# Kernel optimization log

Measured on AMD Instinct MI355X. Metric: run time of the kernel, lower is better.

Reference implementation:

```python
import jax, jax.numpy as jnp
import numpy as np

DIM = 1024
N_QUAT = DIM // 4
LN_EPS = 1e-5
NORM_EPS = 1e-12


def quat_mul(q1, q2):
    # q1, q2: [B, L, N, 4]
    r1, i1, j1, k1 = q1[..., 0], q1[..., 1], q1[..., 2], q1[..., 3]
    r2, i2, j2, k2 = q2[..., 0], q2[..., 1], q2[..., 2], q2[..., 3]
    r = r1 * r2 - i1 * i2 - j1 * j2 - k1 * k2
    i = r1 * i2 + i1 * r2 + j1 * k2 - k1 * j2
    j = r1 * j2 - i1 * k2 + j1 * r2 + k1 * i2
    k = r1 * k2 + i1 * j2 - j1 * i2 + k1 * r2
    return jnp.stack([r, i, j, k], axis=-1)


def quat_conj(q):
    return q * jnp.array([1.0, -1.0, -1.0, -1.0], dtype=q.dtype)


def setup_inputs() -> dict:
    key = jax.random.key(0)
    ks = jax.random.split(key, 7)
    B, L, D = 4, 4096, DIM
    s = 1.0 / np.sqrt(D)
    return {
        "x": jax.random.normal(ks[0], (B, L, D), dtype=jnp.float32),
        "Wk": jax.random.normal(ks[1], (D, D), dtype=jnp.float32) * s,
        "bk": jnp.zeros((D,), dtype=jnp.float32),
        "Wv": jax.random.normal(ks[2], (D, D), dtype=jnp.float32) * s,
        "bv": jnp.zeros((D,), dtype=jnp.float32),
        "ln_g": jnp.ones((D,), dtype=jnp.float32),
        "ln_b": jnp.zeros((D,), dtype=jnp.float32),
        "Wo": jax.random.normal(ks[3], (D, D), dtype=jnp.float32) * s,
        "bo": jnp.zeros((D,), dtype=jnp.float32),
    }


def reference(x, Wk, bk, Wv, bv, ln_g, ln_b, Wo, bo):
    B, L, D = x.shape
    keys = (x @ Wk.T + bk).reshape(B, L, N_QUAT, 4)
    knorm = jnp.linalg.norm(keys, axis=-1, keepdims=True)
    keys = keys / jnp.maximum(knorm, NORM_EPS)  # F.normalize
    values = (x @ Wv.T + bv).reshape(B, L, N_QUAT, 4)
    bound = quat_mul(values, keys)
    memory = jnp.cumsum(bound, axis=1)
    retrieved = quat_mul(memory, quat_conj(keys)).reshape(B, L, D)
    positions = jnp.arange(1, L + 1, dtype=x.dtype)
    retrieved = retrieved / jnp.sqrt(positions)[None, :, None]
    # LayerNorm over last dim
    mu = jnp.mean(retrieved, axis=-1, keepdims=True)
    var = jnp.var(retrieved, axis=-1, keepdims=True)
    normed = (retrieved - mu) / jnp.sqrt(var + LN_EPS) * ln_g + ln_b
    return x + (normed @ Wo.T + bo)
```

## Files before the change

kernel.cpp:

```cpp
#include <hip/hip_runtime.h>
#include <cstdint>
#include <cstddef>


typedef float    f32x4 __attribute__((ext_vector_type(4)));
typedef _Float16 f16x8 __attribute__((ext_vector_type(8)));
typedef _Float16 f16x4 __attribute__((ext_vector_type(4)));

#define DEV static __device__ __forceinline__

constexpr int BATCH = 4;
constexpr int LSEQ  = 4096;
constexpr int DIMN  = 1024;
constexpr int MROW  = BATCH * LSEQ;
constexpr int SEG   = 128;
constexpr int SL    = LSEQ / SEG;
constexpr int NT    = DIMN / 64;

DEV f32x4 qmul(f32x4 a, f32x4 b) {
  f32x4 r;
  r.x = a.x*b.x - a.y*b.y - a.z*b.z - a.w*b.w;
  r.y = a.x*b.y + a.y*b.x + a.z*b.w - a.w*b.z;
  r.z = a.x*b.z - a.y*b.w + a.z*b.x + a.w*b.y;
  r.w = a.x*b.w + a.y*b.z - a.z*b.y + a.w*b.x;
  return r;
}

DEV f32x4 h2f(f16x4 h) {
  return (f32x4){(float)h.x, (float)h.y, (float)h.z, (float)h.w};
}

__global__ __launch_bounds__(256) void k_cast_all(
    const float* __restrict__ x, const float* __restrict__ w0,
    const float* __restrict__ w1, const float* __restrict__ w2,
    _Float16* __restrict__ out) {
  const int XN4 = MROW * DIMN / 4;
  const int WN4 = DIMN * DIMN / 4;
  int i = blockIdx.x * 256 + threadIdx.x;
  if (i >= XN4 + 3 * WN4) return;
  const float* src; int j;
  if (i < XN4)                { src = x;  j = i; }
  else if (i < XN4 + WN4)     { src = w0; j = i - XN4; }
  else if (i < XN4 + 2 * WN4) { src = w1; j = i - XN4 - WN4; }
  else                        { src = w2; j = i - XN4 - 2 * WN4; }
  f32x4 v = ((const f32x4*)src)[j];
  f16x4 o = { (_Float16)v.x, (_Float16)v.y, (_Float16)v.z, (_Float16)v.w };
  ((f16x4*)out)[i] = o;
}

__global__ __launch_bounds__(512, 2) void k_gemm256(
    const _Float16* __restrict__ A, const _Float16* __restrict__ Bw,
    const float* __restrict__ biasA, const float* __restrict__ biasB, int nsplit,
    _Float16* __restrict__ C, int ldC, int nbn) {
  extern __shared__ char smem[];
  const int tid  = threadIdx.x;
  const int lane = tid & 63;
  const int wid  = tid >> 6;
  const int wr = wid >> 2, wc = wid & 3;

  const int nwg = gridDim.x;
  const int cpx = nwg >> 3;
  const int swz = (blockIdx.x & 7) * cpx + (blockIdx.x >> 3);
  const int bm = swz / nbn, bn = swz % nbn;

  auto regBase = [](int slot, int isB, int half) -> unsigned {
    return (unsigned)(((slot * 2 + isB) * 2 + half) * 16384);
  };
  const int r8    = lane >> 3;
  const int sslot = (lane & 7) ^ r8;
  const char* aT = (const char*)(A  + (size_t)bm * 256 * DIMN);
  const char* bT = (const char*)(Bw + (size_t)bn * 256 * DIMN);

  auto stage = [&](int isB, int half, int slot, int kt) {
    const char* gb = (isB ? bT : aT) + (size_t)(half * 128) * 2048 + kt * 128;
    const unsigned reg = regBase(slot, isB, half);
#pragma unroll
    for (int i = 0; i < 2; ++i) {
      const int c = wid * 2 + i;
      const char* src = gb + (size_t)(c * 8 + r8) * 2048 + (sslot << 4);
      __builtin_amdgcn_global_load_lds(
          (const __attribute__((address_space(1))) void*)src,
          (__attribute__((address_space(3))) void*)(smem + reg + c * 1024), 16, 0, 0);
    }
  };
  auto fragA = [&](int slot, int m, int kk) -> f16x8 {
    const int half = m >> 2;
    const int row  = wr * 64 + (m & 3) * 16 + (lane & 15);
    const int sl   = (kk * 4 + (lane >> 4)) ^ (row & 7);
    return *(const f16x8*)(smem + regBase(slot, 0, half) + row * 128 + (sl << 4));
  };
  auto fragB = [&](int slot, int n, int kk) -> f16x8 {
    const int half = n >> 1;
    const int row  = wc * 32 + (n & 1) * 16 + (lane & 15);
    const int sl   = (kk * 4 + (lane >> 4)) ^ (row & 7);
    return *(const f16x8*)(smem + regBase(slot, 1, half) + row * 128 + (sl << 4));
  };

  f32x4 acc[8][4];
#pragma unroll
  for (int m = 0; m < 8; ++m)
#pragma unroll
    for (int n = 0; n < 4; ++n) acc[m][n] = (f32x4){0.f, 0.f, 0.f, 0.f};

  stage(0, 0, 0, 0); stage(1, 0, 0, 0); stage(0, 1, 0, 0); stage(1, 1, 0, 0);

  f16x8 a[4][2], b[4][2];
#pragma unroll 2
  for (int T = 0; T < NT; ++T) {
    const int slot = T & 1, ns = slot ^ 1;
    const bool pf = (T + 1 < NT);
    if (pf) {
      stage(0, 0, ns, T + 1); stage(1, 0, ns, T + 1);
      stage(0, 1, ns, T + 1); stage(1, 1, ns, T + 1);
      asm volatile("s_waitcnt vmcnt(8)" ::: "memory");
    } else {
      asm volatile("s_waitcnt vmcnt(0)" ::: "memory");
    }
    __builtin_amdgcn_s_barrier();

#pragma unroll
    for (int m = 0; m < 4; ++m) { a[m][0] = fragA(slot, m, 0); a[m][1] = fragA(slot, m, 1); }
#pragma unroll
    for (int n = 0; n < 4; ++n) { b[n][0] = fragB(slot, n, 0); b[n][1] = fragB(slot, n, 1); }
    __builtin_amdgcn_s_setprio(1);
#pragma unroll
    for (int m = 0; m < 4; ++m)
#pragma unroll
      for (int n = 0; n < 4; ++n) {
        acc[m][n] = __builtin_amdgcn_mfma_f32_16x16x32_f16(a[m][0], b[n][0], acc[m][n], 0, 0, 0);
        acc[m][n] = __builtin_amdgcn_mfma_f32_16x16x32_f16(a[m][1], b[n][1], acc[m][n], 0, 0, 0);
      }
    __builtin_amdgcn_s_setprio(0);

#pragma unroll
    for (int m = 0; m < 4; ++m) { a[m][0] = fragA(slot, m + 4, 0); a[m][1] = fragA(slot, m + 4, 1); }
    __builtin_amdgcn_s_setprio(1);
#pragma unroll
    for (int m = 0; m < 4; ++m)
#pragma unroll
      for (int n = 0; n < 4; ++n) {
        acc[m + 4][n] = __builtin_amdgcn_mfma_f32_16x16x32_f16(a[m][0], b[n][0], acc[m + 4][n], 0, 0, 0);
        acc[m + 4][n] = __builtin_amdgcn_mfma_f32_16x16x32_f16(a[m][1], b[n][1], acc[m + 4][n], 0, 0, 0);
      }
    __builtin_amdgcn_s_setprio(0);
    __builtin_amdgcn_s_barrier();
  }

  const int r0 = bm * 256 + wr * 64 + ((lane >> 4) << 2);
  const int c0 = bn * 256 + wc * 32 + (lane & 15);
#pragma unroll
  for (int n = 0; n < 4; ++n) {
    const int col = c0 + (n >> 1) * 128 + (n & 1) * 16;
    const float bc = (col < nsplit) ? biasA[col] : biasB[col - nsplit];
#pragma unroll
    for (int m = 0; m < 8; ++m) {
      const int row = r0 + (m >> 2) * 128 + (m & 3) * 16;
#pragma unroll
      for (int t = 0; t < 4; ++t) {
        C[(size_t)(row + t) * ldC + col] = (_Float16)(acc[m][n][t] + bc);
      }
    }
  }
}

__global__ __launch_bounds__(512, 2) void k_gemm_out(
    const _Float16* __restrict__ A, const _Float16* __restrict__ Bw,
    const float* __restrict__ bias, const _Float16* __restrict__ residH,
    float* __restrict__ C, int nbn) {
  extern __shared__ char smem[];
  const int tid  = threadIdx.x;
  const int lane = tid & 63;
  const int wid  = tid >> 6;
  const int wr = wid >> 2, wc = wid & 3;

  const int nwg = gridDim.x;
  const int cpx = nwg >> 3;
  const int swz = (blockIdx.x & 7) * cpx + (blockIdx.x >> 3);
  const int bm = swz / nbn, bn = swz % nbn;

  const int r8    = lane >> 3;
  const int sslot = (lane & 7) ^ r8;
  const char* aT = (const char*)(A  + (size_t)bm * 128 * DIMN);
  const char* bT = (const char*)(Bw + (size_t)bn * 256 * DIMN);

  auto stage3 = [&](int slot, int kt) {
    char* base = smem + slot * 49152;
#pragma unroll
    for (int i = 0; i < 2; ++i) {
      const int c = wid * 2 + i;
      const char* src = aT + kt * 128 + (size_t)(c * 8 + r8) * 2048 + (sslot << 4);
      __builtin_amdgcn_global_load_lds(
          (const __attribute__((address_space(1))) void*)src,
          (__attribute__((address_space(3))) void*)(base + c * 1024), 16, 0, 0);
    }
#pragma unroll
    for (int i = 0; i < 4; ++i) {
      const int c = wid * 4 + i;
      const char* src = bT + kt * 128 + (size_t)(c * 8 + r8) * 2048 + (sslot << 4);
      __builtin_amdgcn_global_load_lds(
          (const __attribute__((address_space(1))) void*)src,
          (__attribute__((address_space(3))) void*)(base + 16384 + c * 1024), 16, 0, 0);
    }
  };
  auto fragA = [&](int slot, int m, int kk) -> f16x8 {
    const int row = wr * 64 + m * 16 + (lane & 15);
    const int sl  = (kk * 4 + (lane >> 4)) ^ (row & 7);
    return *(const f16x8*)(smem + slot * 49152 + row * 128 + (sl << 4));
  };
  auto fragB = [&](int slot, int n, int kk) -> f16x8 {
    const int row = (n >> 1) * 128 + wc * 32 + (n & 1) * 16 + (lane & 15);
    const int sl  = (kk * 4 + (lane >> 4)) ^ (row & 7);
    return *(const f16x8*)(smem + slot * 49152 + 16384 + row * 128 + (sl << 4));
  };

  f32x4 acc[4][4];
#pragma unroll
  for (int m = 0; m < 4; ++m)
#pragma unroll
    for (int n = 0; n < 4; ++n) acc[m][n] = (f32x4){0.f, 0.f, 0.f, 0.f};

  stage3(0, 0); stage3(1, 1);

  f16x8 a[4][2], b[4][2];
  for (int T = 0; T < NT; ++T) {
    const int s = T % 3, sw = (T + 2) % 3;
    if (T + 2 < NT) {
      stage3(sw, T + 2);
      asm volatile("s_waitcnt vmcnt(6)" ::: "memory");
    } else {
      asm volatile("s_waitcnt vmcnt(0)" ::: "memory");
    }
    __builtin_amdgcn_s_barrier();
#pragma unroll
    for (int m = 0; m < 4; ++m) { a[m][0] = fragA(s, m, 0); a[m][1] = fragA(s, m, 1); }
#pragma unroll
    for (int n = 0; n < 4; ++n) { b[n][0] = fragB(s, n, 0); b[n][1] = fragB(s, n, 1); }
    __builtin_amdgcn_s_setprio(1);
#pragma unroll
    for (int m = 0; m < 4; ++m)
#pragma unroll
      for (int n = 0; n < 4; ++n) {
        acc[m][n] = __builtin_amdgcn_mfma_f32_16x16x32_f16(a[m][0], b[n][0], acc[m][n], 0, 0, 0);
        acc[m][n] = __builtin_amdgcn_mfma_f32_16x16x32_f16(a[m][1], b[n][1], acc[m][n], 0, 0, 0);
      }
    __builtin_amdgcn_s_setprio(0);
    __builtin_amdgcn_s_barrier();
  }

  const int r0 = bm * 128 + wr * 64 + ((lane >> 4) << 2);
  const int c0 = bn * 256 + wc * 32 + (lane & 15);
#pragma unroll
  for (int n = 0; n < 4; ++n) {
    const int col = c0 + (n >> 1) * 128 + (n & 1) * 16;
    const float bc = bias[col];
#pragma unroll
    for (int m = 0; m < 4; ++m) {
      const int row = r0 + m * 16;
#pragma unroll
      for (int t = 0; t < 4; ++t) {
        const size_t off = (size_t)(row + t) * DIMN + col;
        C[off] = acc[m][n][t] + bc + (float)residH[off];
      }
    }
  }
}

__global__ __launch_bounds__(256) void k_segsum(const _Float16* __restrict__ KVh,
                                                float* __restrict__ segsum) {
  const int b = blockIdx.x >> 7, seg = blockIdx.x & 127, n = threadIdx.x;
  f32x4 ssum = (f32x4){0.f, 0.f, 0.f, 0.f};
  const size_t rb = (size_t)(b * LSEQ + seg * SL) * 2048 + n * 4;
  for (int l = 0; l < SL; ++l) {
    const size_t p = rb + (size_t)l * 2048;
    f32x4 kq = h2f(*(const f16x4*)(KVh + p));
    f32x4 vq = h2f(*(const f16x4*)(KVh + p + 1024));
    float nn = sqrtf(kq.x*kq.x + kq.y*kq.y + kq.z*kq.z + kq.w*kq.w);
    f32x4 kh = kq * (1.0f / fmaxf(nn, 1e-12f));
    ssum += qmul(vq, kh);
  }
  ((f32x4*)segsum)[(size_t)blockIdx.x * 256 + n] = ssum;
}

__global__ __launch_bounds__(256) void k_segscan(const float* __restrict__ segsum,
                                                 float* __restrict__ segoff) {
  const int gt = blockIdx.x * 256 + threadIdx.x;
  const int b = gt >> 10, ch = gt & 1023;
  float run = 0.f;
  for (int s = 0; s < SEG; ++s) {
    const size_t idx = ((size_t)(b * SEG + s)) * 1024 + ch;
    float v = segsum[idx];
    segoff[idx] = run;
    run += v;
  }
}

__global__ __launch_bounds__(256) void k_retrieve_ln(
    const _Float16* __restrict__ KVh, const float* __restrict__ segoff,
    const float* __restrict__ g, const float* __restrict__ bb,
    _Float16* __restrict__ out) {
  const int b = blockIdx.x >> 7, seg = blockIdx.x & 127, n = threadIdx.x;
  const int wid = n >> 6, lane = n & 63;
  __shared__ float p1[2][4], p2[2][4];
  f32x4 mem = ((const f32x4*)segoff)[(size_t)blockIdx.x * 256 + n];
  const f32x4 gg  = ((const f32x4*)g)[n];
  const f32x4 bvv = ((const f32x4*)bb)[n];
  const size_t rb = (size_t)(b * LSEQ + seg * SL) * 2048 + n * 4;
  const int grow = b * LSEQ + seg * SL;

  f16x4 kq = *(const f16x4*)(KVh + rb);
  f16x4 vq = *(const f16x4*)(KVh + rb + 1024);
  for (int l = 0; l < SL; ++l) {
    f16x4 kqn, vqn;
    if (l + 1 < SL) {
      kqn = *(const f16x4*)(KVh + rb + (size_t)(l + 1) * 2048);
      vqn = *(const f16x4*)(KVh + rb + (size_t)(l + 1) * 2048 + 1024);
    }
    f32x4 kf = h2f(kq), vf = h2f(vq);
    float nn = sqrtf(kf.x*kf.x + kf.y*kf.y + kf.z*kf.z + kf.w*kf.w);
    f32x4 kh = kf * (1.0f / fmaxf(nn, 1e-12f));
    mem += qmul(vf, kh);
    f32x4 kc = (f32x4){kh.x, -kh.y, -kh.z, -kh.w};
    f32x4 r = qmul(mem, kc);
    r *= rsqrtf((float)(seg * SL + l + 1));

    float s1 = r.x + r.y + r.z + r.w;
    float s2 = r.x*r.x + r.y*r.y + r.z*r.z + r.w*r.w;
#pragma unroll
    for (int off = 32; off > 0; off >>= 1) {
      s1 += __shfl_down(s1, off, 64);
      s2 += __shfl_down(s2, off, 64);
    }
    if (lane == 0) { p1[l & 1][wid] = s1; p2[l & 1][wid] = s2; }
    __syncthreads();
    const float ts1 = p1[l & 1][0] + p1[l & 1][1] + p1[l & 1][2] + p1[l & 1][3];
    const float ts2 = p2[l & 1][0] + p2[l & 1][1] + p2[l & 1][2] + p2[l & 1][3];
    const float mu = ts1 * (1.0f / 1024.0f);
    const float var = ts2 * (1.0f / 1024.0f) - mu * mu;
    const float rstd = rsqrtf(var + 1e-5f);
    f32x4 nv = (r - mu) * rstd * gg + bvv;
    f16x4 o = { (_Float16)nv.x, (_Float16)nv.y, (_Float16)nv.z, (_Float16)nv.w };
    ((f16x4*)out)[(size_t)(grow + l) * 256 + n] = o;
    kq = kqn; vq = vqn;
  }
}

extern "C" void kernel_launch(void* const* d_in, const int* in_sizes, int n_in,
                              void* d_out, int out_size, void* d_ws, size_t ws_size,
                              hipStream_t stream) {
  const float* x    = (const float*)d_in[0];
  const float* Wk   = (const float*)d_in[1];
  const float* bk   = (const float*)d_in[2];
  const float* Wv   = (const float*)d_in[3];
  const float* bv   = (const float*)d_in[4];
  const float* ln_g = (const float*)d_in[5];
  const float* ln_b = (const float*)d_in[6];
  const float* Wo   = (const float*)d_in[7];
  const float* bo   = (const float*)d_in[8];
  float* out = (float*)d_out;

  char* ws = (char*)d_ws;
  size_t off = 0;
  auto alloc = [&](size_t bytes) -> void* {
    void* p = ws + off;
    off += (bytes + 255) & ~(size_t)255;
    return p;
  };
  _Float16* xb   = (_Float16*)alloc((size_t)MROW * DIMN * 2);
  _Float16* wkvb = (_Float16*)alloc((size_t)3 * DIMN * DIMN * 2);
  _Float16* KVh  = (_Float16*)alloc((size_t)MROW * 2 * DIMN * 2);
  float* segsum  = (float*)alloc((size_t)BATCH * SEG * DIMN * 4);
  float* segoff  = (float*)alloc((size_t)BATCH * SEG * DIMN * 4);
  _Float16* nb   = (_Float16*)alloc((size_t)MROW * DIMN * 2);
  _Float16* wob  = wkvb + (size_t)2 * DIMN * DIMN;
  (void)off; (void)ws_size; (void)in_sizes; (void)n_in; (void)out_size;

  hipFuncSetAttribute((const void*)k_gemm256,
                      hipFuncAttributeMaxDynamicSharedMemorySize, 131072);
  hipFuncSetAttribute((const void*)k_gemm_out,
                      hipFuncAttributeMaxDynamicSharedMemorySize, 147456);

  const int castN4 = MROW * DIMN / 4 + 3 * DIMN * DIMN / 4;
  k_cast_all<<<(castN4 + 255) / 256, 256, 0, stream>>>(x, Wk, Wv, Wo, xb);

  k_gemm256<<<(MROW / 256) * (2048 / 256), 512, 131072, stream>>>(
      xb, wkvb, bk, bv, 1024, KVh, 2048, 2048 / 256);

  k_segsum<<<BATCH * SEG, 256, 0, stream>>>(KVh, segsum);
  k_segscan<<<BATCH * DIMN / 256, 256, 0, stream>>>(segsum, segoff);
  k_retrieve_ln<<<BATCH * SEG, 256, 0, stream>>>(KVh, segoff, ln_g, ln_b, nb);

  k_gemm_out<<<(MROW / 128) * (DIMN / 256), 512, 147456, stream>>>(
      nb, wob, bo, xb, out, DIMN / 256);
}
```

Measured before the change: 209.8 us.

## Split GEMM prefetch around MFMA halves and fold segment scan into retrieval

The first GEMM now issues half of the next tile's global loads before the first MFMA half and the other half between the two MFMA halves, so the wait only covers the first half's loads. The output GEMM moves its two-ahead prefetch after the fragment reads and replaces the modulo slot indices with rotating counters. The separate segment-scan kernel is removed: each retrieval block sums the preceding segment sums itself. This drops one launch and the segoff buffer, at the cost of redundant prefix reads (up to 127 vectors per thread) in the retrieval kernel.

```diff
diff --git a/kernel.cpp b/kernel.cpp
--- a/kernel.cpp
+++ b/kernel.cpp
@@ -102,7 +102,7 @@
 #pragma unroll
     for (int n = 0; n < 4; ++n) acc[m][n] = (f32x4){0.f, 0.f, 0.f, 0.f};
 
-  stage(0, 0, 0, 0); stage(1, 0, 0, 0); stage(0, 1, 0, 0); stage(1, 1, 0, 0);
+  stage(0, 0, 0, 0); stage(0, 1, 0, 0); stage(1, 0, 0, 0); stage(1, 1, 0, 0);
 
   f16x8 a[4][2], b[4][2];
 #pragma unroll 2
@@ -110,9 +110,8 @@
     const int slot = T & 1, ns = slot ^ 1;
     const bool pf = (T + 1 < NT);
     if (pf) {
-      stage(0, 0, ns, T + 1); stage(1, 0, ns, T + 1);
-      stage(0, 1, ns, T + 1); stage(1, 1, ns, T + 1);
-      asm volatile("s_waitcnt vmcnt(8)" ::: "memory");
+      stage(0, 0, ns, T + 1); stage(0, 1, ns, T + 1);
+      asm volatile("s_waitcnt vmcnt(4)" ::: "memory");
     } else {
       asm volatile("s_waitcnt vmcnt(0)" ::: "memory");
     }
@@ -131,6 +130,8 @@
         acc[m][n] = __builtin_amdgcn_mfma_f32_16x16x32_f16(a[m][1], b[n][1], acc[m][n], 0, 0, 0);
       }
     __builtin_amdgcn_s_setprio(0);
+
+    if (pf) { stage(1, 0, ns, T + 1); stage(1, 1, ns, T + 1); }
 
 #pragma unroll
     for (int m = 0; m < 4; ++m) { a[m][0] = fragA(slot, m + 4, 0); a[m][1] = fragA(slot, m + 4, 1); }
@@ -222,19 +223,16 @@
   stage3(0, 0); stage3(1, 1);
 
   f16x8 a[4][2], b[4][2];
+  int s = 0, sw = 2;
   for (int T = 0; T < NT; ++T) {
-    const int s = T % 3, sw = (T + 2) % 3;
-    if (T + 2 < NT) {
-      stage3(sw, T + 2);
-      asm volatile("s_waitcnt vmcnt(6)" ::: "memory");
-    } else {
-      asm volatile("s_waitcnt vmcnt(0)" ::: "memory");
-    }
+    if (T + 1 < NT) asm volatile("s_waitcnt vmcnt(6)" ::: "memory");
+    else            asm volatile("s_waitcnt vmcnt(0)" ::: "memory");
     __builtin_amdgcn_s_barrier();
 #pragma unroll
     for (int m = 0; m < 4; ++m) { a[m][0] = fragA(s, m, 0); a[m][1] = fragA(s, m, 1); }
 #pragma unroll
     for (int n = 0; n < 4; ++n) { b[n][0] = fragB(s, n, 0); b[n][1] = fragB(s, n, 1); }
+    if (T + 2 < NT) stage3(sw, T + 2);
     __builtin_amdgcn_s_setprio(1);
 #pragma unroll
     for (int m = 0; m < 4; ++m)
@@ -245,6 +243,8 @@
       }
     __builtin_amdgcn_s_setprio(0);
     __builtin_amdgcn_s_barrier();
+    s = (s == 2) ? 0 : s + 1;
+    sw = (sw == 2) ? 0 : sw + 1;
   }
 
   const int r0 = bm * 128 + wr * 64 + ((lane >> 4) << 2);
@@ -281,27 +281,26 @@
   ((f32x4*)segsum)[(size_t)blockIdx.x * 256 + n] = ssum;
 }
 
-__global__ __launch_bounds__(256) void k_segscan(const float* __restrict__ segsum,
-                                                 float* __restrict__ segoff) {
-  const int gt = blockIdx.x * 256 + threadIdx.x;
-  const int b = gt >> 10, ch = gt & 1023;
-  float run = 0.f;
-  for (int s = 0; s < SEG; ++s) {
-    const size_t idx = ((size_t)(b * SEG + s)) * 1024 + ch;
-    float v = segsum[idx];
-    segoff[idx] = run;
-    run += v;
-  }
-}
-
 __global__ __launch_bounds__(256) void k_retrieve_ln(
-    const _Float16* __restrict__ KVh, const float* __restrict__ segoff,
+    const _Float16* __restrict__ KVh, const float* __restrict__ segsum,
     const float* __restrict__ g, const float* __restrict__ bb,
     _Float16* __restrict__ out) {
   const int b = blockIdx.x >> 7, seg = blockIdx.x & 127, n = threadIdx.x;
   const int wid = n >> 6, lane = n & 63;
   __shared__ float p1[2][4], p2[2][4];
-  f32x4 mem = ((const f32x4*)segoff)[(size_t)blockIdx.x * 256 + n];
+
+  f32x4 m0 = (f32x4){0.f, 0.f, 0.f, 0.f}, m1 = (f32x4){0.f, 0.f, 0.f, 0.f};
+  {
+    const f32x4* ss = (const f32x4*)segsum + (size_t)b * SEG * 256 + n;
+    int s = 0;
+    for (; s + 2 <= seg; s += 2) {
+      m0 += ss[(size_t)s * 256];
+      m1 += ss[(size_t)(s + 1) * 256];
+    }
+    if (s < seg) m0 += ss[(size_t)s * 256];
+  }
+  f32x4 mem = m0 + m1;
+
   const f32x4 gg  = ((const f32x4*)g)[n];
   const f32x4 bvv = ((const f32x4*)bb)[n];
   const size_t rb = (size_t)(b * LSEQ + seg * SL) * 2048 + n * 4;
@@ -369,7 +368,6 @@
   _Float16* wkvb = (_Float16*)alloc((size_t)3 * DIMN * DIMN * 2);
   _Float16* KVh  = (_Float16*)alloc((size_t)MROW * 2 * DIMN * 2);
   float* segsum  = (float*)alloc((size_t)BATCH * SEG * DIMN * 4);
-  float* segoff  = (float*)alloc((size_t)BATCH * SEG * DIMN * 4);
   _Float16* nb   = (_Float16*)alloc((size_t)MROW * DIMN * 2);
   _Float16* wob  = wkvb + (size_t)2 * DIMN * DIMN;
   (void)off; (void)ws_size; (void)in_sizes; (void)n_in; (void)out_size;
@@ -386,8 +384,7 @@
       xb, wkvb, bk, bv, 1024, KVh, 2048, 2048 / 256);
 
   k_segsum<<<BATCH * SEG, 256, 0, stream>>>(KVh, segsum);
-  k_segscan<<<BATCH * DIMN / 256, 256, 0, stream>>>(segsum, segoff);
-  k_retrieve_ln<<<BATCH * SEG, 256, 0, stream>>>(KVh, segoff, ln_g, ln_b, nb);
+  k_retrieve_ln<<<BATCH * SEG, 256, 0, stream>>>(KVh, segsum, ln_g, ln_b, nb);
 
   k_gemm_out<<<(MROW / 128) * (DIMN / 256), 512, 147456, stream>>>(
       nb, wob, bo, xb, out, DIMN / 256);
```

Measured after the change: 209.7 us. About the same (-0.0%).
